# Kernel tuning notes

Measured on AMD Instinct MI355X. Metric: run time of the kernel, lower is better.

## Reference

```python
import jax, jax.numpy as jnp
import numpy as np

N_NODES = 100000
N_EDGES = 1600000
D_IN = 128
D_HID = 128
NUM_GRAPHS = 256


def setup_inputs() -> dict:
    key = jax.random.key(0)
    ks = jax.random.split(key, 8)
    x = jax.random.normal(ks[0], (N_NODES, D_IN), dtype=jnp.float32)
    edge_index = jax.random.randint(ks[1], (2, N_EDGES), 0, N_NODES, dtype=jnp.int64)
    batch = jnp.sort(jax.random.randint(ks[2], (N_NODES,), 0, NUM_GRAPHS, dtype=jnp.int64))
    s1 = 1.0 / np.sqrt(D_IN)
    s2 = 1.0 / np.sqrt(D_HID)
    W1 = jax.random.uniform(ks[3], (D_IN, D_HID), jnp.float32, -s1, s1)
    b1 = jnp.zeros((D_HID,), jnp.float32)
    W2 = jax.random.uniform(ks[4], (D_HID, D_HID), jnp.float32, -s2, s2)
    b2 = jnp.zeros((D_HID,), jnp.float32)
    Wm = jax.random.uniform(ks[5], (D_HID, 1), jnp.float32, -s2, s2)
    bm = jnp.zeros((1,), jnp.float32)
    return {"x": x, "edge_index": edge_index, "batch": batch,
            "W1": W1, "b1": b1, "W2": W2, "b2": b2, "Wm": Wm, "bm": bm}


def _gcn_norm(edge_index, n_nodes):
    # add self loops, then symmetric normalization deg^-1/2 * A_hat * deg^-1/2
    loops = jnp.arange(n_nodes, dtype=edge_index.dtype)
    src = jnp.concatenate([edge_index[0], loops])  # [E+N]
    dst = jnp.concatenate([edge_index[1], loops])
    deg = jax.ops.segment_sum(jnp.ones_like(dst, dtype=jnp.float32), dst,
                              num_segments=n_nodes)
    dinv = jnp.where(deg > 0, jax.lax.rsqrt(deg), 0.0)
    norm = dinv[src] * dinv[dst]  # [E+N]
    return src, dst, norm


def _gcn_conv(x, W, b, src, dst, norm, n_nodes):
    h = x @ W                                   # [N, Dout]
    msg = h[src] * norm[:, None]                # gather + scale, [E+N, Dout]
    out = jax.ops.segment_sum(msg, dst, num_segments=n_nodes)  # scatter-add
    return out + b


def reference(x, edge_index, batch, W1, b1, W2, b2, Wm, bm):
    n = x.shape[0]
    src, dst, norm = _gcn_norm(edge_index, n)
    h = _gcn_conv(x, W1, b1, src, dst, norm, n)
    h = jax.nn.relu(h)
    # F.dropout(training=self.training): identity in eval mode
    h = _gcn_conv(h, W2, b2, src, dst, norm, n)
    # global mean pool over graphs
    sums = jax.ops.segment_sum(h, batch, num_segments=NUM_GRAPHS)
    cnt = jax.ops.segment_sum(jnp.ones((n,), h.dtype), batch, num_segments=NUM_GRAPHS)
    pooled = sums / jnp.maximum(cnt, 1.0)[:, None]   # [G, Dhid]
    return pooled @ Wm + bm                           # [G, 1]
```

## Files before the change

### kernel.cpp

```cpp
#include <hip/hip_runtime.h>
#include <hip/hip_bf16.h>

#define NNODES 100000
#define NEDGES 1600000
#define DF 128
#define NGRAPH 256
#define SCAN_CHUNK 2048
#define NB_SCAN ((NNODES + SCAN_CHUNK - 1) / SCAN_CHUNK)

#define BUCKET_SHIFT 7
#define BUCKET_NODES 128
#define NBUCK ((NNODES + BUCKET_NODES - 1) / BUCKET_NODES)
#define SCHUNK 8192
#define NBLK2 ((NEDGES + SCHUNK - 1) / SCHUNK)

typedef __attribute__((ext_vector_type(8))) short short8;
typedef __attribute__((ext_vector_type(4))) float f32x4;

__global__ __launch_bounds__(1024) void hist2(const int* __restrict__ dst,
                                              int* __restrict__ cnt, int E) {
    __shared__ int h[NBUCK];
    for (int i = threadIdx.x; i < NBUCK; i += 1024) h[i] = 0;
    __syncthreads();
    int base = blockIdx.x * SCHUNK;
    #pragma unroll
    for (int j = 0; j < 8; j++) {
        int e = base + threadIdx.x + j * 1024;
        if (e < E) atomicAdd(&h[dst[e] >> BUCKET_SHIFT], 1);
    }
    __syncthreads();
    for (int i = threadIdx.x; i < NBUCK; i += 1024)
        cnt[blockIdx.x * NBUCK + i] = h[i];
}

__global__ void bscan1(const int* __restrict__ cnt, int* __restrict__ bstart,
                       int* __restrict__ btot) {
    int b = blockIdx.x;
    int l = threadIdx.x;
    int vals[4];
    int s = 0;
    #pragma unroll
    for (int i = 0; i < 4; i++) {
        int blk = l * 4 + i;
        vals[i] = (blk < NBLK2) ? cnt[blk * NBUCK + b] : 0;
        s += vals[i];
    }
    int pre = s;
    for (int off = 1; off < 64; off <<= 1) {
        int t = __shfl_up(pre, off, 64);
        if (l >= off) pre += t;
    }
    pre -= s;
    int run = pre;
    #pragma unroll
    for (int i = 0; i < 4; i++) {
        int blk = l * 4 + i;
        if (blk < NBLK2) { bstart[blk * NBUCK + b] = run; run += vals[i]; }
    }
    if (l == 63) btot[b] = pre + s;
}

__global__ void segscan2(const int* __restrict__ btot, int* __restrict__ segoff) {
    __shared__ int lds[256];
    int t = threadIdx.x;
    int b0 = t * 4;
    int v[4];
    int s = 0;
    #pragma unroll
    for (int i = 0; i < 4; i++) { int b = b0 + i; v[i] = (b < NBUCK) ? btot[b] : 0; s += v[i]; }
    lds[t] = s;
    __syncthreads();
    for (int off = 1; off < 256; off <<= 1) {
        int x = lds[t];
        int a = (t >= off) ? lds[t - off] : 0;
        __syncthreads();
        lds[t] = x + a;
        __syncthreads();
    }
    int run = lds[t] - s;
    #pragma unroll
    for (int i = 0; i < 4; i++) {
        int b = b0 + i;
        if (b < NBUCK) { segoff[b] = run; run += v[i]; }
    }
    if (t == 255) segoff[NBUCK] = lds[255];
}

__global__ __launch_bounds__(1024) void scatter2(const int* __restrict__ src,
                                                 const int* __restrict__ dst,
                                                 const int* __restrict__ bstart,
                                                 const int* __restrict__ segoff,
                                                 unsigned int* __restrict__ stage, int E) {
    __shared__ unsigned int rec[SCHUNK];
    __shared__ unsigned short bid[SCHUNK];
    __shared__ int hs[1024];
    __shared__ int cur[NBUCK];
    __shared__ int delta[NBUCK];
    int tid = threadIdx.x;
    int base = blockIdx.x * SCHUNK;
    hs[tid] = 0;
    __syncthreads();
    int myd[8], mys[8];
    #pragma unroll
    for (int j = 0; j < 8; j++) {
        int e = base + tid + j * 1024;
        if (e < E) {
            myd[j] = dst[e];
            mys[j] = src[e];
            atomicAdd(&hs[myd[j] >> BUCKET_SHIFT], 1);
        } else myd[j] = -1;
    }
    __syncthreads();
    int cnt_t = hs[tid];
    for (int off = 1; off < 1024; off <<= 1) {
        int x = hs[tid];
        int a = (tid >= off) ? hs[tid - off] : 0;
        __syncthreads();
        hs[tid] = x + a;
        __syncthreads();
    }
    int excl = hs[tid] - cnt_t;
    if (tid < NBUCK) {
        cur[tid] = excl;
        delta[tid] = segoff[tid] + bstart[blockIdx.x * NBUCK + tid] - excl;
    }
    __syncthreads();
    #pragma unroll
    for (int j = 0; j < 8; j++) {
        if (myd[j] >= 0) {
            int b = myd[j] >> BUCKET_SHIFT;
            int p = atomicAdd(&cur[b], 1);
            rec[p] = (unsigned int)mys[j] | (((unsigned int)myd[j] & 127u) << 17);
            bid[p] = (unsigned short)b;
        }
    }
    __syncthreads();
    int nrec = hs[1023];
    for (int i = tid; i < nrec; i += 1024)
        stage[delta[bid[i]] + i] = rec[i];
}

__global__ void bucket_deg(const unsigned int* __restrict__ stage, const int* __restrict__ segoff,
                           int* __restrict__ deg, int n) {
    __shared__ int h[BUCKET_NODES];
    int b = blockIdx.x;
    if (threadIdx.x < BUCKET_NODES) h[threadIdx.x] = 0;
    __syncthreads();
    int s0 = segoff[b], s1 = segoff[b + 1];
    for (int i = s0 + threadIdx.x; i < s1; i += 256)
        atomicAdd(&h[(stage[i] >> 17) & 127u], 1);
    __syncthreads();
    int v = b * BUCKET_NODES + threadIdx.x;
    if (threadIdx.x < BUCKET_NODES && v < n) deg[v] = h[threadIdx.x];
}

__global__ void scan1_kernel(const int* __restrict__ deg, int* __restrict__ psum,
                             float* __restrict__ dinv, int n) {
    __shared__ int lds[256];
    int t = threadIdx.x;
    int base = blockIdx.x * SCAN_CHUNK + t * 8;
    int s = 0;
    #pragma unroll
    for (int i = 0; i < 8; i++) {
        int idx = base + i;
        if (idx < n) {
            int d = deg[idx];
            dinv[idx] = rsqrtf((float)d + 1.0f);
            s += d + 1;
        }
    }
    lds[t] = s;
    __syncthreads();
    for (int off = 128; off > 0; off >>= 1) {
        if (t < off) lds[t] += lds[t + off];
        __syncthreads();
    }
    if (t == 0) psum[blockIdx.x] = lds[0];
}

__global__ void scan2_kernel(int* __restrict__ psum, int* __restrict__ offs, int nb, int n) {
    __shared__ int lds[64];
    int t = threadIdx.x;
    int v = (t < nb) ? psum[t] : 0;
    lds[t] = v;
    __syncthreads();
    for (int off = 1; off < 64; off <<= 1) {
        int x = lds[t];
        int add = (t >= off) ? lds[t - off] : 0;
        __syncthreads();
        lds[t] = x + add;
        __syncthreads();
    }
    if (t < nb) psum[t] = lds[t] - v;
    if (t == 63) offs[n] = lds[63];
}

__global__ void scan3_kernel(const int* __restrict__ deg, const int* __restrict__ psum,
                             int* __restrict__ offs, int n) {
    __shared__ int lds[256];
    int t = threadIdx.x;
    int base = blockIdx.x * SCAN_CHUNK + t * 8;
    int dv[8];
    int s = 0;
    #pragma unroll
    for (int i = 0; i < 8; i++) {
        int idx = base + i;
        dv[i] = (idx < n) ? deg[idx] + 1 : 0;
        s += dv[i];
    }
    lds[t] = s;
    __syncthreads();
    for (int off = 1; off < 256; off <<= 1) {
        int x = lds[t];
        int add = (t >= off) ? lds[t - off] : 0;
        __syncthreads();
        lds[t] = x + add;
        __syncthreads();
    }
    int run = psum[blockIdx.x] + lds[t] - s;
    #pragma unroll
    for (int i = 0; i < 8; i++) {
        int idx = base + i;
        if (idx < n) { offs[idx] = run; run += dv[i]; }
    }
}

__global__ void bucket_place(const unsigned int* __restrict__ stage, const int* __restrict__ segoff,
                             const int* __restrict__ offs, int* __restrict__ csrc, int n) {
    __shared__ int cur[BUCKET_NODES];
    int b = blockIdx.x;
    int v = b * BUCKET_NODES + threadIdx.x;
    if (threadIdx.x < BUCKET_NODES && v < n) {
        int o = offs[v];
        csrc[o] = v;
        cur[threadIdx.x] = o + 1;
    }
    __syncthreads();
    int s0 = segoff[b], s1 = segoff[b + 1];
    for (int i = s0 + threadIdx.x; i < s1; i += 256) {
        unsigned int r = stage[i];
        int pos = atomicAdd(&cur[(r >> 17) & 127u], 1);
        csrc[pos] = (int)(r & 0x1ffffu);
    }
}

__device__ __forceinline__ unsigned int pack_bf16x2(float a, float b) {
    unsigned int ua = __float_as_uint(a);
    unsigned int ub = __float_as_uint(b);
    ua += 0x7fffu + ((ua >> 16) & 1u);
    ub += 0x7fffu + ((ub >> 16) & 1u);
    return (ua >> 16) | (ub & 0xffff0000u);
}

__device__ __forceinline__ void split_bf16(float w, unsigned short& h, unsigned short& l) {
    unsigned int uw = __float_as_uint(w);
    unsigned int hb = uw + 0x7fffu + ((uw >> 16) & 1u);
    h = (unsigned short)(hb >> 16);
    float rem = w - __uint_as_float((unsigned int)h << 16);
    unsigned int ur = __float_as_uint(rem);
    unsigned int lb = ur + 0x7fffu + ((ur >> 16) & 1u);
    l = (unsigned short)(lb >> 16);
}

__global__ void wprep_kernel(const float* __restrict__ W, unsigned short* __restrict__ Wh,
                             unsigned short* __restrict__ Wl) {
    int id = blockIdx.x * 256 + threadIdx.x;
    if (id >= 2048) return;
    int lane = id & 63, tq = id >> 6;
    int t = tq >> 2, q = tq & 3;
    int n = 16 * t + (lane & 15);
    int kbase = 32 * q + 8 * (lane >> 4);
    unsigned short h[8], l[8];
    #pragma unroll
    for (int i = 0; i < 8; i++) {
        split_bf16(W[(kbase + i) * DF + n], h[i], l[i]);
    }
    uint4 hv, lv;
    hv.x = h[0] | ((unsigned int)h[1] << 16); hv.y = h[2] | ((unsigned int)h[3] << 16);
    hv.z = h[4] | ((unsigned int)h[5] << 16); hv.w = h[6] | ((unsigned int)h[7] << 16);
    lv.x = l[0] | ((unsigned int)l[1] << 16); lv.y = l[2] | ((unsigned int)l[3] << 16);
    lv.z = l[4] | ((unsigned int)l[5] << 16); lv.w = l[6] | ((unsigned int)l[7] << 16);
    ((uint4*)Wh)[id] = hv;
    ((uint4*)Wl)[id] = lv;
}

template <int ABF16>
__global__ void gemm_mfma(const void* __restrict__ Ap, const unsigned short* __restrict__ Wh,
                          const unsigned short* __restrict__ Wl, const float* __restrict__ dinv,
                          unsigned int* __restrict__ C, int nrows) {
    int tid = threadIdx.x;
    int wv = tid >> 6, lane = tid & 63;
    int c16 = lane & 15, g = lane >> 4;
    int row = blockIdx.x * 64 + wv * 16 + c16;
    int rowc = min(row, nrows - 1);
    const short8* Wh8 = (const short8*)Wh;
    const short8* Wl8 = (const short8*)Wl;
    f32x4 acc[8];
    #pragma unroll
    for (int t = 0; t < 8; t++) acc[t] = (f32x4){0.f, 0.f, 0.f, 0.f};
    #pragma unroll
    for (int q = 0; q < 4; q++) {
        short8 ah, al;
        if (ABF16) {
            ah = ((const short8*)Ap)[(size_t)rowc * 16 + q * 4 + g];
        } else {
            const float4* A4 = (const float4*)Ap;
            float4 a0 = A4[(size_t)rowc * 32 + q * 8 + g * 2];
            float4 a1 = A4[(size_t)rowc * 32 + q * 8 + g * 2 + 1];
            float av[8] = {a0.x, a0.y, a0.z, a0.w, a1.x, a1.y, a1.z, a1.w};
            #pragma unroll
            for (int i = 0; i < 8; i++) {
                unsigned short hs, ls;
                split_bf16(av[i], hs, ls);
                ah[i] = (short)hs;
                al[i] = (short)ls;
            }
        }
        #pragma unroll
        for (int t = 0; t < 8; t++) {
            short8 wh = Wh8[(t * 4 + q) * 64 + lane];
            short8 wl = Wl8[(t * 4 + q) * 64 + lane];
            acc[t] = __builtin_amdgcn_mfma_f32_16x16x32_bf16(wh, ah, acc[t], 0, 0, 0);
            if (!ABF16) acc[t] = __builtin_amdgcn_mfma_f32_16x16x32_bf16(wh, al, acc[t], 0, 0, 0);
            acc[t] = __builtin_amdgcn_mfma_f32_16x16x32_bf16(wl, ah, acc[t], 0, 0, 0);
        }
    }
    if (row < nrows) {
        float dvr = dinv[row];
        uint2* C2 = (uint2*)C;
        #pragma unroll
        for (int t = 0; t < 8; t++) {
            uint2 w;
            w.x = pack_bf16x2(acc[t][0] * dvr, acc[t][1] * dvr);
            w.y = pack_bf16x2(acc[t][2] * dvr, acc[t][3] * dvr);
            C2[(size_t)row * 32 + t * 4 + g] = w;
        }
    }
}

template <int BIAS_RELU, int OUT16>
__global__ void agg_kernel(const int* __restrict__ roff, const int* __restrict__ csrc,
                           const float* __restrict__ dinv, const unsigned int* __restrict__ Hb,
                           const float* __restrict__ bias, void* __restrict__ Out) {
    int tid = threadIdx.x;
    int wv = tid >> 6, lane = tid & 63;
    size_t v = (size_t)blockIdx.x * 4 + wv;
    int b = roff[v], e = roff[v + 1];
    float2 acc = {0.f, 0.f};
    for (int base = b; base < e; base += 64) {
        int idx = base + lane;
        if (idx >= e) idx = e - 1;
        int rec = csrc[idx];
        int kmax = min(64, e - base);
        int k = 0;
        for (; k + 8 <= kmax; k += 8) {
            unsigned int u[8];
            #pragma unroll
            for (int j = 0; j < 8; j++) {
                int s = __shfl(rec, k + j, 64);
                u[j] = Hb[(size_t)s * 64 + lane];
            }
            #pragma unroll
            for (int j = 0; j < 8; j++) {
                acc.x += __uint_as_float(u[j] << 16);
                acc.y += __uint_as_float(u[j] & 0xffff0000u);
            }
        }
        for (; k < kmax; k++) {
            int s0 = __shfl(rec, k, 64);
            unsigned int u0 = Hb[(size_t)s0 * 64 + lane];
            acc.x += __uint_as_float(u0 << 16);
            acc.y += __uint_as_float(u0 & 0xffff0000u);
        }
    }
    float dvv = dinv[v];
    acc.x *= dvv;
    acc.y *= dvv;
    if (BIAS_RELU) {
        float2 bb = ((const float2*)bias)[lane];
        acc.x = fmaxf(acc.x + bb.x, 0.f);
        acc.y = fmaxf(acc.y + bb.y, 0.f);
    }
    if (OUT16) {
        ((unsigned int*)Out)[v * 64 + lane] = pack_bf16x2(acc.x, acc.y);
    } else {
        ((float2*)Out)[v * 64 + lane] = acc;
    }
}

__global__ void pool_kernel(const float* __restrict__ H, const int* __restrict__ batch,
                            float* __restrict__ gsum, float* __restrict__ gcnt, int n) {
    __shared__ int bl[128];
    int d = threadIdx.x;
    int base = blockIdx.x * 128;
    int cnt_here = min(128, n - base);
    if (cnt_here <= 0) return;
    if (d < cnt_here) bl[d] = batch[base + d];
    __syncthreads();
    float acc = 0.f;
    int cg = -1, c = 0;
    for (int i = 0; i < cnt_here; i++) {
        int g = bl[i];
        if (g != cg) {
            if (cg >= 0) {
                atomicAdd(&gsum[cg * DF + d], acc);
                if (d == 0) atomicAdd(&gcnt[cg], (float)c);
            }
            acc = 0.f; c = 0; cg = g;
        }
        acc += H[(size_t)(base + i) * DF + d];
        c++;
    }
    if (cg >= 0) {
        atomicAdd(&gsum[cg * DF + d], acc);
        if (d == 0) atomicAdd(&gcnt[cg], (float)c);
    }
}

__global__ void final_kernel(const float* __restrict__ gsum, const float* __restrict__ gcnt,
                             const float* __restrict__ b2, const float* __restrict__ Wm,
                             const float* __restrict__ bm, float* __restrict__ out) {
    __shared__ float red[2];
    int g = blockIdx.x, d = threadIdx.x;
    float cnt = fmaxf(gcnt[g], 1.0f);
    float v = (gsum[g * DF + d] / cnt + b2[d]) * Wm[d];
    for (int off = 32; off > 0; off >>= 1) v += __shfl_down(v, off, 64);
    if ((d & 63) == 0) red[d >> 6] = v;
    __syncthreads();
    if (d == 0) out[g] = red[0] + red[1] + bm[0];
}

extern "C" void kernel_launch(void* const* d_in, const int* in_sizes, int n_in,
                              void* d_out, int out_size, void* d_ws, size_t ws_size,
                              hipStream_t stream) {
    const float* x   = (const float*)d_in[0];
    const int*   ei  = (const int*)d_in[1];
    const int*   bat = (const int*)d_in[2];
    const float* W1  = (const float*)d_in[3];
    const float* b1  = (const float*)d_in[4];
    const float* W2  = (const float*)d_in[5];
    const float* b2  = (const float*)d_in[6];
    const float* Wm  = (const float*)d_in[7];
    const float* bm  = (const float*)d_in[8];
    float* out = (float*)d_out;

    const int N = NNODES, E = NEDGES, G = NGRAPH;
    const int* src = ei;
    const int* dst = ei + E;

    char* base = (char*)d_ws;
    size_t o = 0;
    auto alloc = [&](size_t bytes) { size_t p = o; o = (o + bytes + 255) & ~(size_t)255; return p; };
    int*   deg    = (int*)(base + alloc((size_t)N * 4));
    int*   offs   = (int*)(base + alloc((size_t)(N + 1) * 4));
    float* dinv   = (float*)(base + alloc((size_t)N * 4));
    int*   psum   = (int*)(base + alloc((size_t)NB_SCAN * 4));
    int*   cnt    = (int*)(base + alloc((size_t)NBLK2 * NBUCK * 4));
    int*   bstart = (int*)(base + alloc((size_t)NBLK2 * NBUCK * 4));
    int*   btot   = (int*)(base + alloc((size_t)NBUCK * 4));
    int*   segoff = (int*)(base + alloc((size_t)(NBUCK + 1) * 4));
    unsigned int* stage = (unsigned int*)(base + alloc((size_t)E * 4));
    int*   csrc   = (int*)(base + alloc((size_t)(E + N) * 4));
    unsigned int* bufH  = (unsigned int*)(base + alloc((size_t)N * DF * 2));
    unsigned int* bufA16 = (unsigned int*)(base + alloc((size_t)N * DF * 2));
    float* bufB   = (float*)(base + alloc((size_t)N * DF * 4));
    float* gsum   = (float*)(base + alloc((size_t)G * DF * 4));
    float* gcnt   = (float*)(base + alloc((size_t)G * 4));
    unsigned short* wh1 = (unsigned short*)(base + alloc(2048 * 16));
    unsigned short* wl1 = (unsigned short*)(base + alloc(2048 * 16));
    unsigned short* wh2 = (unsigned short*)(base + alloc(2048 * 16));
    unsigned short* wl2 = (unsigned short*)(base + alloc(2048 * 16));
    (void)ws_size;

    hipMemsetAsync(gsum, 0, (size_t)G * DF * 4, stream);
    hipMemsetAsync(gcnt, 0, (size_t)G * 4, stream);

    hist2<<<NBLK2, 1024, 0, stream>>>(dst, cnt, E);
    bscan1<<<NBUCK, 64, 0, stream>>>(cnt, bstart, btot);
    segscan2<<<1, 256, 0, stream>>>(btot, segoff);
    scatter2<<<NBLK2, 1024, 0, stream>>>(src, dst, bstart, segoff, stage, E);
    bucket_deg<<<NBUCK, 256, 0, stream>>>(stage, segoff, deg, N);
    scan1_kernel<<<NB_SCAN, 256, 0, stream>>>(deg, psum, dinv, N);
    scan2_kernel<<<1, 64, 0, stream>>>(psum, offs, NB_SCAN, N);
    scan3_kernel<<<NB_SCAN, 256, 0, stream>>>(deg, psum, offs, N);
    bucket_place<<<NBUCK, 256, 0, stream>>>(stage, segoff, offs, csrc, N);

    wprep_kernel<<<8, 256, 0, stream>>>(W1, wh1, wl1);
    wprep_kernel<<<8, 256, 0, stream>>>(W2, wh2, wl2);

    gemm_mfma<0><<<(N + 63) / 64, 256, 0, stream>>>(x, wh1, wl1, dinv, bufH, N);
    agg_kernel<1, 1><<<N / 4, 256, 0, stream>>>(offs, csrc, dinv, bufH, b1, bufA16);

    gemm_mfma<1><<<(N + 63) / 64, 256, 0, stream>>>(bufA16, wh2, wl2, dinv, bufH, N);
    agg_kernel<0, 0><<<N / 4, 256, 0, stream>>>(offs, csrc, dinv, bufH, nullptr, bufB);

    pool_kernel<<<(N + 127) / 128, 128, 0, stream>>>(bufB, bat, gsum, gcnt, N);
    final_kernel<<<G, 128, 0, stream>>>(gsum, gcnt, b2, Wm, bm, out);
}
```

Before: 284.3 us.

## Fuse pooling into second aggregation, widen gathers, use wave-level scan in scatter

The second aggregation now reduces directly into per-graph sums with atomics, so the fp32 intermediate buffer and the separate pool kernel are no longer needed. Both aggregation kernels gather 8-byte chunks, with each half-wave handling a different neighbor row, and combine the halves with an xor shuffle. The scatter kernel's 1024-step barrier-based Hillis-Steele scan becomes a shuffle scan within each wave plus a 16-entry cross-wave prefix. The two weight-prep launches are merged into one. In exchange, pooling issues many more atomics per node block, with full 128-wide atomics whenever the 4 nodes in a block belong to different graphs.

```diff
diff --git a/kernel.cpp b/kernel.cpp
--- a/kernel.cpp
+++ b/kernel.cpp
@@ -94,9 +94,11 @@
     __shared__ unsigned int rec[SCHUNK];
     __shared__ unsigned short bid[SCHUNK];
     __shared__ int hs[1024];
+    __shared__ int wsum[16];
     __shared__ int cur[NBUCK];
     __shared__ int delta[NBUCK];
-    int tid = threadIdx.x;
+    __shared__ int nrec_s;
+    int tid = threadIdx.x, lane = tid & 63, wid = tid >> 6;
     int base = blockIdx.x * SCHUNK;
     hs[tid] = 0;
     __syncthreads();
@@ -112,14 +114,21 @@
     }
     __syncthreads();
     int cnt_t = hs[tid];
-    for (int off = 1; off < 1024; off <<= 1) {
-        int x = hs[tid];
-        int a = (tid >= off) ? hs[tid - off] : 0;
-        __syncthreads();
-        hs[tid] = x + a;
-        __syncthreads();
-    }
-    int excl = hs[tid] - cnt_t;
+    int pre = cnt_t;
+    for (int off = 1; off < 64; off <<= 1) {
+        int t = __shfl_up(pre, off, 64);
+        if (lane >= off) pre += t;
+    }
+    if (lane == 63) wsum[wid] = pre;
+    __syncthreads();
+    if (tid == 0) {
+        int r = 0;
+        #pragma unroll
+        for (int i = 0; i < 16; i++) { int t = wsum[i]; wsum[i] = r; r += t; }
+        nrec_s = r;
+    }
+    __syncthreads();
+    int excl = pre - cnt_t + wsum[wid];
     if (tid < NBUCK) {
         cur[tid] = excl;
         delta[tid] = segoff[tid] + bstart[blockIdx.x * NBUCK + tid] - excl;
@@ -135,7 +144,7 @@
         }
     }
     __syncthreads();
-    int nrec = hs[1023];
+    int nrec = nrec_s;
     for (int i = tid; i < nrec; i += 1024)
         stage[delta[bid[i]] + i] = rec[i];
 }
@@ -262,10 +271,15 @@
     l = (unsigned short)(lb >> 16);
 }
 
-__global__ void wprep_kernel(const float* __restrict__ W, unsigned short* __restrict__ Wh,
-                             unsigned short* __restrict__ Wl) {
-    int id = blockIdx.x * 256 + threadIdx.x;
-    if (id >= 2048) return;
+__global__ void wprep2(const float* __restrict__ W1, const float* __restrict__ W2,
+                       unsigned short* __restrict__ Wh1, unsigned short* __restrict__ Wl1,
+                       unsigned short* __restrict__ Wh2, unsigned short* __restrict__ Wl2) {
+    int gidx = blockIdx.x * 256 + threadIdx.x;
+    int which = gidx >> 11;
+    int id = gidx & 2047;
+    const float* W = which ? W2 : W1;
+    unsigned short* Wh = which ? Wh2 : Wh1;
+    unsigned short* Wl = which ? Wl2 : Wl1;
     int lane = id & 63, tq = id >> 6;
     int t = tq >> 2, q = tq & 3;
     int n = 16 * t + (lane & 15);
@@ -338,15 +352,13 @@
     }
 }
 
-template <int BIAS_RELU, int OUT16>
-__global__ void agg_kernel(const int* __restrict__ roff, const int* __restrict__ csrc,
-                           const float* __restrict__ dinv, const unsigned int* __restrict__ Hb,
-                           const float* __restrict__ bias, void* __restrict__ Out) {
-    int tid = threadIdx.x;
-    int wv = tid >> 6, lane = tid & 63;
-    size_t v = (size_t)blockIdx.x * 4 + wv;
+__device__ __forceinline__ float4 gather_rows(const int* __restrict__ roff,
+                                              const int* __restrict__ csrc,
+                                              const uint2* __restrict__ H2,
+                                              size_t v, int lane) {
+    int half = lane >> 5, fl = lane & 31;
     int b = roff[v], e = roff[v + 1];
-    float2 acc = {0.f, 0.f};
+    float4 acc = {0.f, 0.f, 0.f, 0.f};
     for (int base = b; base < e; base += 64) {
         int idx = base + lane;
         if (idx >= e) idx = e - 1;
@@ -354,66 +366,96 @@
         int kmax = min(64, e - base);
         int k = 0;
         for (; k + 8 <= kmax; k += 8) {
-            unsigned int u[8];
+            uint2 u[4];
             #pragma unroll
-            for (int j = 0; j < 8; j++) {
-                int s = __shfl(rec, k + j, 64);
-                u[j] = Hb[(size_t)s * 64 + lane];
+            for (int p = 0; p < 4; p++) {
+                int s = __shfl(rec, k + 2 * p + half, 64);
+                u[p] = H2[(size_t)s * 32 + fl];
             }
             #pragma unroll
-            for (int j = 0; j < 8; j++) {
-                acc.x += __uint_as_float(u[j] << 16);
-                acc.y += __uint_as_float(u[j] & 0xffff0000u);
+            for (int p = 0; p < 4; p++) {
+                acc.x += __uint_as_float(u[p].x << 16);
+                acc.y += __uint_as_float(u[p].x & 0xffff0000u);
+                acc.z += __uint_as_float(u[p].y << 16);
+                acc.w += __uint_as_float(u[p].y & 0xffff0000u);
             }
         }
-        for (; k < kmax; k++) {
-            int s0 = __shfl(rec, k, 64);
-            unsigned int u0 = Hb[(size_t)s0 * 64 + lane];
-            acc.x += __uint_as_float(u0 << 16);
-            acc.y += __uint_as_float(u0 & 0xffff0000u);
-        }
-    }
+        for (; k + 2 <= kmax; k += 2) {
+            int s = __shfl(rec, k + half, 64);
+            uint2 u = H2[(size_t)s * 32 + fl];
+            acc.x += __uint_as_float(u.x << 16);
+            acc.y += __uint_as_float(u.x & 0xffff0000u);
+            acc.z += __uint_as_float(u.y << 16);
+            acc.w += __uint_as_float(u.y & 0xffff0000u);
+        }
+        if (k < kmax) {
+            int s = __shfl(rec, k, 64);
+            uint2 u = H2[(size_t)s * 32 + fl];
+            float m = (half == 0) ? 1.0f : 0.0f;
+            acc.x += m * __uint_as_float(u.x << 16);
+            acc.y += m * __uint_as_float(u.x & 0xffff0000u);
+            acc.z += m * __uint_as_float(u.y << 16);
+            acc.w += m * __uint_as_float(u.y & 0xffff0000u);
+        }
+    }
+    acc.x += __shfl_xor(acc.x, 32, 64);
+    acc.y += __shfl_xor(acc.y, 32, 64);
+    acc.z += __shfl_xor(acc.z, 32, 64);
+    acc.w += __shfl_xor(acc.w, 32, 64);
+    return acc;
+}
+
+__global__ void agg_mid(const int* __restrict__ roff, const int* __restrict__ csrc,
+                        const float* __restrict__ dinv, const uint2* __restrict__ H2,
+                        const float* __restrict__ bias, uint2* __restrict__ Out) {
+    int tid = threadIdx.x, wv = tid >> 6, lane = tid & 63;
+    size_t v = (size_t)blockIdx.x * 4 + wv;
+    float4 acc = gather_rows(roff, csrc, H2, v, lane);
     float dvv = dinv[v];
-    acc.x *= dvv;
-    acc.y *= dvv;
-    if (BIAS_RELU) {
-        float2 bb = ((const float2*)bias)[lane];
-        acc.x = fmaxf(acc.x + bb.x, 0.f);
-        acc.y = fmaxf(acc.y + bb.y, 0.f);
-    }
-    if (OUT16) {
-        ((unsigned int*)Out)[v * 64 + lane] = pack_bf16x2(acc.x, acc.y);
+    int fl = lane & 31;
+    if (lane < 32) {
+        float4 bb = ((const float4*)bias)[fl];
+        float a0 = fmaxf(acc.x * dvv + bb.x, 0.f);
+        float a1 = fmaxf(acc.y * dvv + bb.y, 0.f);
+        float a2 = fmaxf(acc.z * dvv + bb.z, 0.f);
+        float a3 = fmaxf(acc.w * dvv + bb.w, 0.f);
+        Out[v * 32 + fl] = make_uint2(pack_bf16x2(a0, a1), pack_bf16x2(a2, a3));
+    }
+}
+
+__global__ void agg_pool(const int* __restrict__ roff, const int* __restrict__ csrc,
+                         const float* __restrict__ dinv, const uint2* __restrict__ H2,
+                         const int* __restrict__ batch,
+                         float* __restrict__ gsum, float* __restrict__ gcnt) {
+    __shared__ float red[4][128];
+    __shared__ int gid[4];
+    __shared__ int same;
+    int tid = threadIdx.x, wv = tid >> 6, lane = tid & 63, fl = lane & 31;
+    size_t v = (size_t)blockIdx.x * 4 + wv;
+    float4 acc = gather_rows(roff, csrc, H2, v, lane);
+    float dvv = dinv[v];
+    acc.x *= dvv; acc.y *= dvv; acc.z *= dvv; acc.w *= dvv;
+    if (lane < 32) *(float4*)&red[wv][fl * 4] = acc;
+    if (lane == 0) gid[wv] = batch[v];
+    __syncthreads();
+    if (tid == 0) same = (gid[0] == gid[1]) && (gid[1] == gid[2]) && (gid[2] == gid[3]);
+    __syncthreads();
+    if (same) {
+        if (wv == 0) {
+            #pragma unroll
+            for (int r = 0; r < 2; r++) {
+                int f = lane + r * 64;
+                atomicAdd(&gsum[gid[0] * DF + f], red[0][f] + red[1][f] + red[2][f] + red[3][f]);
+            }
+            if (lane == 0) atomicAdd(&gcnt[gid[0]], 4.0f);
+        }
     } else {
-        ((float2*)Out)[v * 64 + lane] = acc;
-    }
-}
-
-__global__ void pool_kernel(const float* __restrict__ H, const int* __restrict__ batch,
-                            float* __restrict__ gsum, float* __restrict__ gcnt, int n) {
-    __shared__ int bl[128];
-    int d = threadIdx.x;
-    int base = blockIdx.x * 128;
-    int cnt_here = min(128, n - base);
-    if (cnt_here <= 0) return;
-    if (d < cnt_here) bl[d] = batch[base + d];
-    __syncthreads();
-    float acc = 0.f;
-    int cg = -1, c = 0;
-    for (int i = 0; i < cnt_here; i++) {
-        int g = bl[i];
-        if (g != cg) {
-            if (cg >= 0) {
-                atomicAdd(&gsum[cg * DF + d], acc);
-                if (d == 0) atomicAdd(&gcnt[cg], (float)c);
-            }
-            acc = 0.f; c = 0; cg = g;
-        }
-        acc += H[(size_t)(base + i) * DF + d];
-        c++;
-    }
-    if (cg >= 0) {
-        atomicAdd(&gsum[cg * DF + d], acc);
-        if (d == 0) atomicAdd(&gcnt[cg], (float)c);
+        #pragma unroll
+        for (int r = 0; r < 2; r++) {
+            int f = lane + r * 64;
+            atomicAdd(&gsum[gid[wv] * DF + f], red[wv][f]);
+        }
+        if (lane == 0) atomicAdd(&gcnt[gid[wv]], 1.0f);
     }
 }
 
@@ -463,7 +505,6 @@
     int*   csrc   = (int*)(base + alloc((size_t)(E + N) * 4));
     unsigned int* bufH  = (unsigned int*)(base + alloc((size_t)N * DF * 2));
     unsigned int* bufA16 = (unsigned int*)(base + alloc((size_t)N * DF * 2));
-    float* bufB   = (float*)(base + alloc((size_t)N * DF * 4));
     float* gsum   = (float*)(base + alloc((size_t)G * DF * 4));
     float* gcnt   = (float*)(base + alloc((size_t)G * 4));
     unsigned short* wh1 = (unsigned short*)(base + alloc(2048 * 16));
@@ -485,15 +526,13 @@
     scan3_kernel<<<NB_SCAN, 256, 0, stream>>>(deg, psum, offs, N);
     bucket_place<<<NBUCK, 256, 0, stream>>>(stage, segoff, offs, csrc, N);
 
-    wprep_kernel<<<8, 256, 0, stream>>>(W1, wh1, wl1);
-    wprep_kernel<<<8, 256, 0, stream>>>(W2, wh2, wl2);
+    wprep2<<<16, 256, 0, stream>>>(W1, W2, wh1, wl1, wh2, wl2);
 
     gemm_mfma<0><<<(N + 63) / 64, 256, 0, stream>>>(x, wh1, wl1, dinv, bufH, N);
-    agg_kernel<1, 1><<<N / 4, 256, 0, stream>>>(offs, csrc, dinv, bufH, b1, bufA16);
+    agg_mid<<<N / 4, 256, 0, stream>>>(offs, csrc, dinv, (const uint2*)bufH, b1, (uint2*)bufA16);
 
     gemm_mfma<1><<<(N + 63) / 64, 256, 0, stream>>>(bufA16, wh2, wl2, dinv, bufH, N);
-    agg_kernel<0, 0><<<N / 4, 256, 0, stream>>>(offs, csrc, dinv, bufH, nullptr, bufB);
-
-    pool_kernel<<<(N + 127) / 128, 128, 0, stream>>>(bufB, bat, gsum, gcnt, N);
+    agg_pool<<<N / 4, 256, 0, stream>>>(offs, csrc, dinv, (const uint2*)bufH, bat, gsum, gcnt);
+
     final_kernel<<<G, 128, 0, stream>>>(gsum, gcnt, b2, Wm, bm, out);
 }
```

Result: slower. 313.2 us (+10.1%).
